# Kernel optimization log

Hardware: AMD Instinct MI355X
Metric: run time of the kernel (lower is better)

## Reference

```python
import jax, jax.numpy as jnp
import numpy as np

N, D, H = 8192, 256, 128


def setup_inputs() -> dict:
    key = jax.random.key(0)
    k1, k2, k3, k4 = jax.random.split(key, 4)
    x = jax.random.normal(k1, (N, D), dtype=jnp.float32)
    y = jax.random.normal(k2, (N, D), dtype=jnp.float32)
    W1 = jax.random.normal(k3, (D, H), dtype=jnp.float32) * (1.0 / np.sqrt(D))
    b1 = jnp.zeros((H,), dtype=jnp.float32)
    W2 = jax.random.normal(k4, (H, D), dtype=jnp.float32) * (1.0 / np.sqrt(H))
    b2 = jnp.zeros((D,), dtype=jnp.float32)
    return {"x": x, "y": y, "W1": W1, "b1": b1, "W2": W2, "b2": b2}


def _l2norm(v):
    # torch.nn.functional.normalize(dim=-1): v / max(||v||, eps)
    n = jnp.sqrt(jnp.sum(v * v, axis=-1, keepdims=True))
    return v / jnp.maximum(n, 1e-12)


def _neg_cos_loss_stopgrad(p, z):
    p_n = _l2norm(p)
    z_n = _l2norm(jax.lax.stop_gradient(z))
    return -jnp.mean(jnp.sum(p_n * z_n, axis=1))


def reference(x, y, W1, b1, W2, b2):
    def mlp(v):
        h = jax.nn.relu(v @ W1 + b1)
        return h @ W2 + b2

    p_x = mlp(x)
    p_y = mlp(y)
    loss = 0.5 * (_neg_cos_loss_stopgrad(p_x, y) + _neg_cos_loss_stopgrad(p_y, x))

    # accuracy branch (original naively broadcasts [N,D,1]*[1,D,N]; same math as matmul)
    p_x_n = _l2norm(p_x)
    p_y_n = _l2norm(p_y)
    x_n = _l2norm(x)
    y_n = _l2norm(y)
    sim_x = p_x_n @ y_n.T  # [N, N], sim_x[i, j] = p_x[i] . y[j]
    sim_y = p_y_n @ x_n.T  # [N, N]
    gold = jnp.arange(x.shape[0])
    # NOTE: faithful to original parenthesization: 0.5 * first term + second term
    acc_x = 0.5 * jnp.mean((jnp.argmax(sim_x, axis=0) == gold).astype(jnp.float32)) + \
            jnp.mean((jnp.argmax(sim_x, axis=1) == gold).astype(jnp.float32))
    acc_y = 0.5 * jnp.mean((jnp.argmax(sim_y, axis=0) == gold).astype(jnp.float32)) + \
            jnp.mean((jnp.argmax(sim_y, axis=1) == gold).astype(jnp.float32))
    return loss, acc_x, acc_y
```

## Files before the change

kernel.cpp:

```cpp
#include <hip/hip_runtime.h>


static constexpr int N = 8192;
static constexpr int D = 256;
static constexpr int H = 128;

typedef __attribute__((ext_vector_type(8))) short s16x8;
typedef __attribute__((ext_vector_type(4))) float fp32x4;
typedef unsigned long long ull;

__device__ __forceinline__ unsigned f2ord(float f) {
    unsigned u = __float_as_uint(f);
    return (u & 0x80000000u) ? ~u : (u | 0x80000000u);
}
__device__ __forceinline__ ull umax64(ull a, ull b) { return a > b ? a : b; }
__device__ __forceinline__ unsigned short bf16_rtne(float f) {
    unsigned u = __float_as_uint(f);
    unsigned r = 0x7FFFu + ((u >> 16) & 1u);
    return (unsigned short)((u + r) >> 16);
}
__device__ __forceinline__ float bf_f(unsigned short h) {
    return __uint_as_float((unsigned)h << 16);
}
__device__ __forceinline__ void split_store(float f, unsigned short* h, unsigned short* l) {
    unsigned short hb = bf16_rtne(f);
    *h = hb;
    *l = bf16_rtne(f - bf_f(hb));
}
__device__ __forceinline__ void gload16(const unsigned short* g, void* lds) {
    __builtin_amdgcn_global_load_lds(
        (const __attribute__((address_space(1))) unsigned int*)g,
        (__attribute__((address_space(3))) unsigned int*)lds, 16, 0, 0);
}
__device__ __forceinline__ size_t gidx(int panel, int kt, int kq, int m) {
    return (((size_t)(panel * 8 + kt) * 4 + kq) * 128 + m) * 8;
}

static constexpr int MLP_ROWS = 32;

__global__ __launch_bounds__(256) void prep_kernel(
    const float* __restrict__ x, const float* __restrict__ y,
    const float* __restrict__ W1, const float* __restrict__ b1,
    const float* __restrict__ W2, const float* __restrict__ b2,
    unsigned short* __restrict__ pxh, unsigned short* __restrict__ pxl,
    unsigned short* __restrict__ pyh, unsigned short* __restrict__ pyl,
    unsigned short* __restrict__ xh, unsigned short* __restrict__ xl,
    unsigned short* __restrict__ yh, unsigned short* __restrict__ yl,
    ull* __restrict__ keys, int* __restrict__ cnt, float* __restrict__ diagParts)
{
    const int bid = blockIdx.x;
    const int t = threadIdx.x;

    if (bid < 512) {
        __shared__ float sV[MLP_ROWS][D + 4];
        __shared__ float sH[MLP_ROWS][H + 4];
        __shared__ float sNrm[MLP_ROWS];

        const float* V = (bid < 256) ? x : y;
        unsigned short* Ph = (bid < 256) ? pxh : pyh;
        unsigned short* Pl = (bid < 256) ? pxl : pyl;
        const int rowBase = (bid & 255) * MLP_ROWS;

        for (int i = t; i < MLP_ROWS * (D / 4); i += 256) {
            int r = i >> 6, c4 = i & 63;
            float4 v = *reinterpret_cast<const float4*>(&V[(size_t)(rowBase + r) * D + c4 * 4]);
            sV[r][c4 * 4 + 0] = v.x; sV[r][c4 * 4 + 1] = v.y;
            sV[r][c4 * 4 + 2] = v.z; sV[r][c4 * 4 + 3] = v.w;
        }
        __syncthreads();

        {
            const int c = t & (H - 1);
            const int r0 = (t >> 7) * 16;
            float acc[16];
#pragma unroll
            for (int i = 0; i < 16; ++i) acc[i] = 0.f;
            for (int k4 = 0; k4 < D / 4; ++k4) {
                float w0 = W1[(k4 * 4 + 0) * H + c];
                float w1 = W1[(k4 * 4 + 1) * H + c];
                float w2 = W1[(k4 * 4 + 2) * H + c];
                float w3 = W1[(k4 * 4 + 3) * H + c];
#pragma unroll
                for (int i = 0; i < 16; ++i) {
                    float4 v = *reinterpret_cast<const float4*>(&sV[r0 + i][k4 * 4]);
                    acc[i] = fmaf(v.w, w3, fmaf(v.z, w2, fmaf(v.y, w1, fmaf(v.x, w0, acc[i]))));
                }
            }
            float bb = b1[c];
#pragma unroll
            for (int i = 0; i < 16; ++i) {
                float h = acc[i] + bb;
                sH[r0 + i][c] = h > 0.f ? h : 0.f;
            }
        }
        __syncthreads();

        {
            const int c = t;
            float acc[MLP_ROWS];
#pragma unroll
            for (int i = 0; i < MLP_ROWS; ++i) acc[i] = 0.f;
            for (int k4 = 0; k4 < H / 4; ++k4) {
                float w0 = W2[(k4 * 4 + 0) * D + c];
                float w1 = W2[(k4 * 4 + 1) * D + c];
                float w2 = W2[(k4 * 4 + 2) * D + c];
                float w3 = W2[(k4 * 4 + 3) * D + c];
#pragma unroll
                for (int i = 0; i < MLP_ROWS; ++i) {
                    float4 v = *reinterpret_cast<const float4*>(&sH[i][k4 * 4]);
                    acc[i] = fmaf(v.w, w3, fmaf(v.z, w2, fmaf(v.y, w1, fmaf(v.x, w0, acc[i]))));
                }
            }
            float bb = b2[c];
            __syncthreads();
#pragma unroll
            for (int i = 0; i < MLP_ROWS; ++i) sV[i][c] = acc[i] + bb;
        }
        __syncthreads();

        {
            const int wave = t >> 6, lane = t & 63;
            for (int r = wave; r < MLP_ROWS; r += 4) {
                float s = 0.f;
#pragma unroll
                for (int c = 0; c < D / 64; ++c) {
                    float v = sV[r][lane + c * 64];
                    s = fmaf(v, v, s);
                }
#pragma unroll
                for (int off = 32; off > 0; off >>= 1) s += __shfl_down(s, off);
                if (lane == 0) sNrm[r] = s;
            }
        }
        __syncthreads();

        for (int i = t; i < MLP_ROWS * (D / 4); i += 256) {
            int r = i >> 6, c4 = i & 63;
            float scale = 1.0f / fmaxf(sqrtf(sNrm[r]), 1e-12f);
            ushort4 h, l;
            split_store(sV[r][c4 * 4 + 0] * scale, &h.x, &l.x);
            split_store(sV[r][c4 * 4 + 1] * scale, &h.y, &l.y);
            split_store(sV[r][c4 * 4 + 2] * scale, &h.z, &l.z);
            split_store(sV[r][c4 * 4 + 3] * scale, &h.w, &l.w);
            int grow = rowBase + r;
            size_t g = gidx(grow >> 7, c4 >> 3, (c4 >> 1) & 3, grow & 127) + (size_t)(c4 & 1) * 4;
            *reinterpret_cast<ushort4*>(&Ph[g]) = h;
            *reinterpret_cast<ushort4*>(&Pl[g]) = l;
        }
    } else {
        const int rb = bid - 512;
        if (t < 128) keys[rb * 128 + t] = 0ULL;
        if (bid == 512) {
            if (t < 128) diagParts[t] = 0.f;
            if (t < 4) cnt[t] = 0;
        }
        const int wave = t >> 6, lane = t & 63;
#pragma unroll 1
        for (int i = 0; i < 16; ++i) {
            int gr = rb * 64 + wave * 16 + i;
            const float* V = (gr < N) ? x : y;
            unsigned short* Vh = (gr < N) ? xh : yh;
            unsigned short* Vl = (gr < N) ? xl : yl;
            int row = gr & (N - 1);
            float4 v = *reinterpret_cast<const float4*>(&V[(size_t)row * D + lane * 4]);
            float s = fmaf(v.x, v.x, fmaf(v.y, v.y, fmaf(v.z, v.z, v.w * v.w)));
#pragma unroll
            for (int off = 32; off > 0; off >>= 1) s += __shfl_down(s, off);
            s = __shfl(s, 0);
            float scale = 1.0f / fmaxf(sqrtf(s), 1e-12f);
            ushort4 h, l;
            split_store(v.x * scale, &h.x, &l.x);
            split_store(v.y * scale, &h.y, &l.y);
            split_store(v.z * scale, &h.z, &l.z);
            split_store(v.w * scale, &h.w, &l.w);
            size_t g = gidx(row >> 7, lane >> 3, (lane >> 1) & 3, row & 127) + (size_t)(lane & 1) * 4;
            *reinterpret_cast<ushort4*>(&Vh[g]) = h;
            *reinterpret_cast<ushort4*>(&Vl[g]) = l;
        }
    }
}

__global__ __launch_bounds__(256, 4) void sim_argmax_mfma(
    const unsigned short* __restrict__ Axh, const unsigned short* __restrict__ Axl,
    const unsigned short* __restrict__ Byh, const unsigned short* __restrict__ Byl,
    const unsigned short* __restrict__ Ayh, const unsigned short* __restrict__ Ayl,
    const unsigned short* __restrict__ Bxh, const unsigned short* __restrict__ Bxl,
    ull* __restrict__ keys, float* __restrict__ diagParts)
{
    __shared__ s16x8 sS[4][512];
    __shared__ ull kbufR[128][2];
    __shared__ ull kbufC[128][2];
    __shared__ float sDiag[4];

    const int t = threadIdx.x;
    const int w = t >> 6, lane = t & 63;
    const int wr = w >> 1, wc = w & 1;

    const int bidFull = blockIdx.x;
    const int sim = bidFull >> 12;
    const int bid = bidFull & 4095;

    const unsigned short* Ah = sim ? Ayh : Axh;
    const unsigned short* Al = sim ? Ayl : Axl;
    const unsigned short* Bh = sim ? Bxh : Byh;
    const unsigned short* Bl = sim ? Bxl : Byl;
    ull* rowKeys = keys + (sim ? 2 * N : 0);
    ull* colKeys = keys + (sim ? 3 * N : (size_t)N);
    float* diagP = diagParts + (sim ? 64 : 0);

    const int xcd = bid & 7, local = bid >> 3;
    const int rowTile = (xcd & 3) * 16 + (local & 15);
    const int colTile = (xcd >> 2) * 32 + (local >> 4);
    const int rowBase = rowTile * 128;
    const int colBase = colTile * 128;

    fp32x4 acc[4][4];
#pragma unroll
    for (int i = 0; i < 4; ++i)
#pragma unroll
        for (int j = 0; j < 4; ++j) acc[i][j] = (fp32x4){0.f, 0.f, 0.f, 0.f};

    const unsigned short* pAh = Ah + (size_t)rowTile * 4096 * 8;
    const unsigned short* pAl = Al + (size_t)rowTile * 4096 * 8;
    const unsigned short* pBh = Bh + (size_t)colTile * 4096 * 8;
    const unsigned short* pBl = Bl + (size_t)colTile * 4096 * 8;

#define STAGE(kt)                                                               \
    do {                                                                        \
        const size_t o0 = (size_t)(kt) * 512 + w * 128 + lane;                  \
        const size_t o1 = o0 + 64;                                              \
        gload16(pAh + o0 * 8, (void*)&sS[0][w * 128]);                          \
        gload16(pAh + o1 * 8, (void*)&sS[0][w * 128 + 64]);                     \
        gload16(pAl + o0 * 8, (void*)&sS[1][w * 128]);                          \
        gload16(pAl + o1 * 8, (void*)&sS[1][w * 128 + 64]);                     \
        gload16(pBh + o0 * 8, (void*)&sS[2][w * 128]);                          \
        gload16(pBh + o1 * 8, (void*)&sS[2][w * 128 + 64]);                     \
        gload16(pBl + o0 * 8, (void*)&sS[3][w * 128]);                          \
        gload16(pBl + o1 * 8, (void*)&sS[3][w * 128 + 64]);                     \
    } while (0)

    STAGE(0);

    const int fBase = (lane >> 4) * 128 + (lane & 15);
    const int aBase = fBase + wr * 64;
    const int bBase = fBase + wc * 64;

#pragma unroll 1
    for (int kt = 0; kt < 8; ++kt) {
        __syncthreads();

        s16x8 ah[4], bh[4];
#pragma unroll
        for (int f = 0; f < 4; ++f) ah[f] = sS[0][aBase + f * 16];
#pragma unroll
        for (int f = 0; f < 4; ++f) bh[f] = sS[2][bBase + f * 16];
        __builtin_amdgcn_s_setprio(1);
#pragma unroll
        for (int fm = 0; fm < 4; ++fm)
#pragma unroll
            for (int fn = 0; fn < 4; ++fn)
                acc[fm][fn] = __builtin_amdgcn_mfma_f32_16x16x32_bf16(ah[fm], bh[fn], acc[fm][fn], 0, 0, 0);
        __builtin_amdgcn_s_setprio(0);

        {
            s16x8 al[4];
#pragma unroll
            for (int f = 0; f < 4; ++f) al[f] = sS[1][aBase + f * 16];
            __builtin_amdgcn_s_setprio(1);
#pragma unroll
            for (int fm = 0; fm < 4; ++fm)
#pragma unroll
                for (int fn = 0; fn < 4; ++fn)
                    acc[fm][fn] = __builtin_amdgcn_mfma_f32_16x16x32_bf16(al[fm], bh[fn], acc[fm][fn], 0, 0, 0);
            __builtin_amdgcn_s_setprio(0);
        }
        {
            s16x8 bl[4];
#pragma unroll
            for (int f = 0; f < 4; ++f) bl[f] = sS[3][bBase + f * 16];
            __builtin_amdgcn_s_setprio(1);
#pragma unroll
            for (int fm = 0; fm < 4; ++fm)
#pragma unroll
                for (int fn = 0; fn < 4; ++fn)
                    acc[fm][fn] = __builtin_amdgcn_mfma_f32_16x16x32_bf16(ah[fm], bl[fn], acc[fm][fn], 0, 0, 0);
            __builtin_amdgcn_s_setprio(0);
        }

        __syncthreads();
        if (kt < 7) STAGE(kt + 1);
    }
#undef STAGE

    const int R0 = wr * 64;
    const int C0 = wc * 64;

    if (rowTile == colTile) {
        float s = 0.f;
        if (wr == wc) {
            int dr = (lane & 15) - (lane >> 4) * 4;
            if (dr >= 0 && dr < 4) {
#pragma unroll
                for (int fm = 0; fm < 4; ++fm) s += acc[fm][fm][dr];
            }
        }
#pragma unroll
        for (int off = 32; off > 0; off >>= 1) s += __shfl_down(s, off);
        if (lane == 0) sDiag[w] = s;
        __syncthreads();
        if (t == 0) diagP[rowTile] = ((sDiag[0] + sDiag[1]) + sDiag[2]) + sDiag[3];
    }

#pragma unroll
    for (int fm = 0; fm < 4; ++fm) {
#pragma unroll
        for (int r = 0; r < 4; ++r) {
            int rowLoc = R0 + fm * 16 + (lane >> 4) * 4 + r;
            float m = fmaxf(fmaxf(acc[fm][0][r], acc[fm][1][r]), fmaxf(acc[fm][2][r], acc[fm][3][r]));
#pragma unroll
            for (int off = 1; off < 16; off <<= 1) m = fmaxf(m, __shfl_xor(m, off));
            unsigned idx = 0xFFFFFFFFu;
#pragma unroll
            for (int fn = 0; fn < 4; ++fn) {
                unsigned gcol = (unsigned)(colBase + C0 + fn * 16 + (lane & 15));
                if (acc[fm][fn][r] == m && gcol < idx) idx = gcol;
            }
#pragma unroll
            for (int off = 1; off < 16; off <<= 1) {
                unsigned o = __shfl_xor(idx, off);
                if (o < idx) idx = o;
            }
            if ((lane & 15) == 0)
                kbufR[rowLoc][wc] = ((ull)f2ord(m) << 32) | (unsigned)(~idx);
        }
    }

#pragma unroll
    for (int fn = 0; fn < 4; ++fn) {
        int colLoc = C0 + fn * 16 + (lane & 15);
        float m = -3.4e38f;
#pragma unroll
        for (int fm = 0; fm < 4; ++fm) {
            float m01 = fmaxf(acc[fm][fn][0], acc[fm][fn][1]);
            float m23 = fmaxf(acc[fm][fn][2], acc[fm][fn][3]);
            m = fmaxf(m, fmaxf(m01, m23));
        }
        m = fmaxf(m, __shfl_xor(m, 16));
        m = fmaxf(m, __shfl_xor(m, 32));
        unsigned idx = 0xFFFFFFFFu;
#pragma unroll
        for (int fm = 0; fm < 4; ++fm) {
#pragma unroll
            for (int r = 0; r < 4; ++r) {
                unsigned grow = (unsigned)(rowBase + R0 + fm * 16 + (lane >> 4) * 4 + r);
                if (acc[fm][fn][r] == m && grow < idx) idx = grow;
            }
        }
        {
            unsigned o = __shfl_xor(idx, 16);
            if (o < idx) idx = o;
            o = __shfl_xor(idx, 32);
            if (o < idx) idx = o;
        }
        if ((lane >> 4) == 0)
            kbufC[colLoc][wr] = ((ull)f2ord(m) << 32) | (unsigned)(~idx);
    }

    __syncthreads();

    if (t < 128) {
        ull best = umax64(kbufR[t][0], kbufR[t][1]);
        atomicMax(&rowKeys[rowBase + t], best);
    } else {
        int c = t - 128;
        ull best = umax64(kbufC[c][0], kbufC[c][1]);
        atomicMax(&colKeys[colBase + c], best);
    }
}

__global__ __launch_bounds__(256) void count_kernel(const ull* __restrict__ keys, int* __restrict__ cnt)
{
    const int t = threadIdx.x;
    const int i = blockIdx.x * 256 + t;
    const int lane = t & 63;
#pragma unroll
    for (int a = 0; a < 4; ++a) {
        int s = ((~(unsigned)keys[a * N + i]) == (unsigned)i);
#pragma unroll
        for (int off = 32; off > 0; off >>= 1) s += __shfl_down(s, off);
        if (lane == 0) atomicAdd(&cnt[a], s);
    }
}

__global__ __launch_bounds__(64) void final_kernel(
    const float* __restrict__ diagParts, const int* __restrict__ cnt, float* __restrict__ out)
{
    const int lane = threadIdx.x;
    double vx = (double)diagParts[lane];
    double vy = (double)diagParts[64 + lane];
#pragma unroll
    for (int off = 32; off > 0; off >>= 1) {
        vx += __shfl_down(vx, off);
        vy += __shfl_down(vy, off);
    }
    if (lane == 0) {
        float invN = 1.0f / (float)N;
        out[0] = (float)(-0.5 * (vx + vy) / (double)N);
        out[1] = 0.5f * ((float)cnt[1] * invN) + (float)cnt[0] * invN;
        out[2] = 0.5f * ((float)cnt[3] * invN) + (float)cnt[2] * invN;
    }
}

extern "C" void kernel_launch(void* const* d_in, const int* in_sizes, int n_in,
                              void* d_out, int out_size, void* d_ws, size_t ws_size,
                              hipStream_t stream)
{
    (void)in_sizes; (void)n_in; (void)out_size; (void)ws_size;
    const float* x  = (const float*)d_in[0];
    const float* y  = (const float*)d_in[1];
    const float* W1 = (const float*)d_in[2];
    const float* b1 = (const float*)d_in[3];
    const float* W2 = (const float*)d_in[4];
    const float* b2 = (const float*)d_in[5];
    float* out = (float*)d_out;

    const size_t ND = (size_t)N * D;
    unsigned short* pxh = (unsigned short*)d_ws;
    unsigned short* pxl = pxh + ND;
    unsigned short* pyh = pxl + ND;
    unsigned short* pyl = pyh + ND;
    unsigned short* xh  = pyl + ND;
    unsigned short* xl  = xh + ND;
    unsigned short* yh  = xl + ND;
    unsigned short* yl  = yh + ND;
    ull* keys = (ull*)(yl + ND);
    float* diagParts = (float*)(keys + 4 * N);
    int* cnt = (int*)(diagParts + 128);

    prep_kernel<<<768, 256, 0, stream>>>(x, y, W1, b1, W2, b2,
                                         pxh, pxl, pyh, pyl, xh, xl, yh, yl,
                                         keys, cnt, diagParts);

    sim_argmax_mfma<<<8192, 256, 0, stream>>>(pxh, pxl, yh, yl,
                                              pyh, pyl, xh, xl,
                                              keys, diagParts);

    count_kernel<<<32, 256, 0, stream>>>(keys, cnt);
    final_kernel<<<1, 64, 0, stream>>>(diagParts, cnt, out);
}
```

Before: 283.5 us.

## Load MFMA fragments directly from global memory instead of LDS staging

Removes the LDS staging buffer and block-wide barriers in the similarity GEMM; each wave now loads its bf16 hi/lo fragments directly from the pre-tiled global layout. Launch bounds change from 4 to 3 blocks per CU to allow more registers. This removes barrier and LDS overhead, but each tile is now fetched by two waves through the caches and load latency is no longer overlapped by explicit staging.

```diff
diff --git a/kernel.cpp b/kernel.cpp
--- a/kernel.cpp
+++ b/kernel.cpp
@@ -26,11 +26,6 @@
     unsigned short hb = bf16_rtne(f);
     *h = hb;
     *l = bf16_rtne(f - bf_f(hb));
-}
-__device__ __forceinline__ void gload16(const unsigned short* g, void* lds) {
-    __builtin_amdgcn_global_load_lds(
-        (const __attribute__((address_space(1))) unsigned int*)g,
-        (__attribute__((address_space(3))) unsigned int*)lds, 16, 0, 0);
 }
 __device__ __forceinline__ size_t gidx(int panel, int kt, int kq, int m) {
     return (((size_t)(panel * 8 + kt) * 4 + kq) * 128 + m) * 8;
@@ -180,14 +175,13 @@
     }
 }
 
-__global__ __launch_bounds__(256, 4) void sim_argmax_mfma(
+__global__ __launch_bounds__(256, 3) void sim_argmax_mfma(
     const unsigned short* __restrict__ Axh, const unsigned short* __restrict__ Axl,
     const unsigned short* __restrict__ Byh, const unsigned short* __restrict__ Byl,
     const unsigned short* __restrict__ Ayh, const unsigned short* __restrict__ Ayl,
     const unsigned short* __restrict__ Bxh, const unsigned short* __restrict__ Bxl,
     ull* __restrict__ keys, float* __restrict__ diagParts)
 {
-    __shared__ s16x8 sS[4][512];
     __shared__ ull kbufR[128][2];
     __shared__ ull kbufC[128][2];
     __shared__ float sDiag[4];
@@ -220,40 +214,21 @@
 #pragma unroll
         for (int j = 0; j < 4; ++j) acc[i][j] = (fp32x4){0.f, 0.f, 0.f, 0.f};
 
-    const unsigned short* pAh = Ah + (size_t)rowTile * 4096 * 8;
-    const unsigned short* pAl = Al + (size_t)rowTile * 4096 * 8;
-    const unsigned short* pBh = Bh + (size_t)colTile * 4096 * 8;
-    const unsigned short* pBl = Bl + (size_t)colTile * 4096 * 8;
-
-#define STAGE(kt)                                                               \
-    do {                                                                        \
-        const size_t o0 = (size_t)(kt) * 512 + w * 128 + lane;                  \
-        const size_t o1 = o0 + 64;                                              \
-        gload16(pAh + o0 * 8, (void*)&sS[0][w * 128]);                          \
-        gload16(pAh + o1 * 8, (void*)&sS[0][w * 128 + 64]);                     \
-        gload16(pAl + o0 * 8, (void*)&sS[1][w * 128]);                          \
-        gload16(pAl + o1 * 8, (void*)&sS[1][w * 128 + 64]);                     \
-        gload16(pBh + o0 * 8, (void*)&sS[2][w * 128]);                          \
-        gload16(pBh + o1 * 8, (void*)&sS[2][w * 128 + 64]);                     \
-        gload16(pBl + o0 * 8, (void*)&sS[3][w * 128]);                          \
-        gload16(pBl + o1 * 8, (void*)&sS[3][w * 128 + 64]);                     \
-    } while (0)
-
-    STAGE(0);
-
-    const int fBase = (lane >> 4) * 128 + (lane & 15);
-    const int aBase = fBase + wr * 64;
-    const int bBase = fBase + wc * 64;
+    const int fOff = (lane >> 4) * 128 + (lane & 15);
+    const unsigned short* aH = Ah + ((size_t)rowTile * 4096 + fOff + wr * 64) * 8;
+    const unsigned short* aL = Al + ((size_t)rowTile * 4096 + fOff + wr * 64) * 8;
+    const unsigned short* bH = Bh + ((size_t)colTile * 4096 + fOff + wc * 64) * 8;
+    const unsigned short* bL = Bl + ((size_t)colTile * 4096 + fOff + wc * 64) * 8;
+
+#define FRAG(base, kt, f) (*reinterpret_cast<const s16x8*>((base) + ((size_t)(kt) * 512 + (f) * 16) * 8))
 
 #pragma unroll 1
     for (int kt = 0; kt < 8; ++kt) {
-        __syncthreads();
-
         s16x8 ah[4], bh[4];
 #pragma unroll
-        for (int f = 0; f < 4; ++f) ah[f] = sS[0][aBase + f * 16];
-#pragma unroll
-        for (int f = 0; f < 4; ++f) bh[f] = sS[2][bBase + f * 16];
+        for (int f = 0; f < 4; ++f) ah[f] = FRAG(aH, kt, f);
+#pragma unroll
+        for (int f = 0; f < 4; ++f) bh[f] = FRAG(bH, kt, f);
         __builtin_amdgcn_s_setprio(1);
 #pragma unroll
         for (int fm = 0; fm < 4; ++fm)
@@ -265,7 +240,7 @@
         {
             s16x8 al[4];
 #pragma unroll
-            for (int f = 0; f < 4; ++f) al[f] = sS[1][aBase + f * 16];
+            for (int f = 0; f < 4; ++f) al[f] = FRAG(aL, kt, f);
             __builtin_amdgcn_s_setprio(1);
 #pragma unroll
             for (int fm = 0; fm < 4; ++fm)
@@ -277,7 +252,7 @@
         {
             s16x8 bl[4];
 #pragma unroll
-            for (int f = 0; f < 4; ++f) bl[f] = sS[3][bBase + f * 16];
+            for (int f = 0; f < 4; ++f) bl[f] = FRAG(bL, kt, f);
             __builtin_amdgcn_s_setprio(1);
 #pragma unroll
             for (int fm = 0; fm < 4; ++fm)
@@ -286,11 +261,8 @@
                     acc[fm][fn] = __builtin_amdgcn_mfma_f32_16x16x32_bf16(ah[fm], bl[fn], acc[fm][fn], 0, 0, 0);
             __builtin_amdgcn_s_setprio(0);
         }
-
-        __syncthreads();
-        if (kt < 7) STAGE(kt + 1);
-    }
-#undef STAGE
+    }
+#undef FRAG
 
     const int R0 = wr * 64;
     const int C0 = wc * 64;
```

After: 292.1 us. 3.0% more time.
